# Optimization experiments

Hardware: AMD Instinct MI355X
Metric: run time of the kernel (lower is better)

The kernel has to match this reference:

```python
import jax, jax.numpy as jnp
import numpy as np

B = 32
NC = 10
EPS = 1e-5

# TensorConvLayer2d is modeled as: spatial kh x kw conv over the (H,W)=(32,32) map,
# where each kernel tap applies a bilinear inner-tensor transform U @ T @ V
# (U: [out_t, in_t] on rows, V: [in_t, out_t] on cols), summed over in_channels,
# plus an inner-tensor bias. out_type=0 (fcn_head) contracts the inner tensor to a
# scalar per pixel per output class. TensorBatchNorm2d(18*18) normalizes each of the
# 324 inner-tensor positions over (batch, H, W) with affine gamma/beta (train-mode stats).

def bn(x, g, b):
    # x: (B,H,W,18,18); stats over (B,H,W) per inner position
    m = jnp.mean(x, axis=(0, 1, 2), keepdims=True)
    v = jnp.var(x, axis=(0, 1, 2), keepdims=True)
    return g * (x - m) * jax.lax.rsqrt(v + EPS) + b

def prelu(x, a):
    return jnp.where(x >= 0, x, a * x)

def conv1x1(x, U, V, b):
    # x: (B,H,W,18,18); U,V,b: (18,18)
    return jnp.einsum('bhwpq,ap,qd->bhwad', x, U, V) + b

def conv3x3(x, U, V, b):
    # x: (B,H,W,18,18); U,V: (3,3,18,18); b: (18,18); pad=1, stride=1 on (H,W)
    H, W = x.shape[1], x.shape[2]
    xp = jnp.pad(x, ((0, 0), (1, 1), (1, 1), (0, 0), (0, 0)))
    acc = 0.0
    for i in range(3):
        for j in range(3):
            acc = acc + jnp.einsum('bhwpq,ap,qd->bhwad', xp[:, i:i + H, j:j + W], U[i, j], V[i, j])
    return acc + b

def conv_f0(x, U0, V0, b0):
    # x: (B,8,H,W,16,16) -> (B,H,W,18,18); U0: (8,3,3,18,16), V0: (8,3,3,16,18)
    H, W = x.shape[2], x.shape[3]
    xp = jnp.pad(x, ((0, 0), (0, 0), (1, 1), (1, 1), (0, 0), (0, 0)))
    acc = 0.0
    for i in range(3):
        for j in range(3):
            acc = acc + jnp.einsum('bchwpq,cap,cqd->bhwad', xp[:, :, i:i + H, j:j + W], U0[:, i, j], V0[:, i, j])
    return acc + b0

def _forward(x, U0, V0, b0, U1, V1, b1, U3, V3, b3, Wf, bf, gamma, beta, alpha):
    x = x.reshape(-1, 8, 16, 16, 32, 32).transpose(0, 1, 4, 5, 2, 3)  # (B,8,32,32,16,16)
    h = prelu(bn(conv_f0(x, U0, V0, b0), gamma[0], beta[0]), alpha[0])  # f0

    def resblock(h, i1, i3, ibn, ia):
        t = prelu(bn(conv1x1(h, U1[i1], V1[i1], b1[i1]), gamma[ibn], beta[ibn]), alpha[ia])
        t = prelu(bn(conv3x3(t, U3[i3], V3[i3], b3[i3]), gamma[ibn + 1], beta[ibn + 1]), alpha[ia + 1])
        t = bn(conv1x1(t, U1[i1 + 1], V1[i1 + 1], b1[i1 + 1]), gamma[ibn + 2], beta[ibn + 2])
        return t

    identity = bn(conv1x1(h, U1[0], V1[0], b1[0]), gamma[1], beta[1])      # s1
    x11 = resblock(h, 1, 0, 2, 1) + identity                                # block11
    identity = bn(conv1x1(x11, U1[3], V1[3], b1[3]), gamma[5], beta[5])    # s2
    x21 = resblock(x11, 4, 1, 6, 3) + identity                              # block21
    _dentity = bn(conv1x1(x21, U1[6], V1[6], b1[6]), gamma[9], beta[9])    # s3: typo in source -> unused
    x31 = resblock(x21, 7, 2, 10, 5) + identity                             # bug-faithful: reuses s2 identity
    out = jnp.einsum('bhwpq,opq->bohw', x31, Wf) + bf[None, :, None, None]  # fcn_head, out_type=0
    return out  # (B, NC, 32, 32)

def setup_inputs():
    key = jax.random.key(0)
    ks = jax.random.split(key, 12)
    s = 0.1
    return dict(
        x=jax.random.normal(ks[0], (B, 8, 16, 16, 32, 32), jnp.float32),
        U0=jax.random.normal(ks[1], (8, 3, 3, 18, 16), jnp.float32) * s,
        V0=jax.random.normal(ks[2], (8, 3, 3, 16, 18), jnp.float32) * s,
        b0=jax.random.normal(ks[3], (18, 18), jnp.float32) * s,
        U1=jax.random.normal(ks[4], (9, 18, 18), jnp.float32) * s,
        V1=jax.random.normal(ks[5], (9, 18, 18), jnp.float32) * s,
        b1=jax.random.normal(ks[6], (9, 18, 18), jnp.float32) * s,
        U3=jax.random.normal(ks[7], (3, 3, 3, 18, 18), jnp.float32) * s,
        V3=jax.random.normal(ks[8], (3, 3, 3, 18, 18), jnp.float32) * s,
        b3=jax.random.normal(ks[9], (3, 18, 18), jnp.float32) * s,
        Wf=jax.random.normal(ks[10], (NC, 18, 18), jnp.float32) * s,
        bf=jnp.zeros((NC,), jnp.float32),
        gamma=jnp.ones((13, 18, 18), jnp.float32),
        beta=jnp.zeros((13, 18, 18), jnp.float32),
        alpha=jnp.full((7,), 0.25, jnp.float32),
    )

def reference(x, U0, V0, b0, U1, V1, b1, U3, V3, b3, Wf, bf, gamma, beta, alpha):
    return _forward(x, U0, V0, b0, U1, V1, b1, U3, V3, b3, Wf, bf, gamma, beta, alpha)
```

## Files before the change

kernel.cpp:

```cpp
#include <hip/hip_runtime.h>


#define NPOS 324
#define NPIX 32768
#define NELEM 10616832
#define NF4   2654208

typedef __attribute__((ext_vector_type(8))) short short8;
typedef __attribute__((ext_vector_type(4))) float f32x4;
typedef __attribute__((ext_vector_type(4))) unsigned short us4;

#define AS1 __attribute__((address_space(1)))
#define AS3 __attribute__((address_space(3)))

__device__ __forceinline__ void atomicAddF(float* p, float v) {
    __hip_atomic_fetch_add(p, v, __ATOMIC_RELAXED, __HIP_MEMORY_SCOPE_AGENT);
}
__device__ __forceinline__ unsigned short f2b(float f) {
    unsigned u = __builtin_bit_cast(unsigned, f);
    u = u + 0x7fffu + ((u >> 16) & 1u);
    return (unsigned short)(u >> 16);
}

__global__ __launch_bounds__(512, 2) void k_gconv(
    const unsigned short* __restrict__ in,
    const unsigned short* __restrict__ W,
    float* __restrict__ out,
    float* __restrict__ stats,
    const unsigned short* __restrict__ zb,
    const int KS, const int Kper, const int ntaps)
{
    __shared__ __align__(16) unsigned short Ab[8192];
    __shared__ __align__(16) unsigned short Bb[21504];
    __shared__ float slds[672];

    const int tid = threadIdx.x;
    const int wv  = tid >> 6;
    const int L   = tid & 63;
    const int q   = L >> 4;
    const int l15 = L & 15;
    const int wm  = wv >> 2;
    const int wn  = wv & 3;
    const int ntcnt = (wn == 0) ? 6 : 5;
    const int nt0   = (wn == 0) ? 0 : 6 + 5 * (wn - 1);

    const int blk  = blockIdx.x;
    const int pix0 = blk * 128;
    const int b    = blk >> 3;
    const int h0   = (blk & 7) * 4;

    for (int i = tid; i < 672; i += 512) slds[i] = 0.f;

    const f32x4 fzero = {0.f, 0.f, 0.f, 0.f};
    f32x4 acc[4][6];
#pragma unroll
    for (int i = 0; i < 4; ++i)
#pragma unroll
        for (int j = 0; j < 6; ++j) acc[i][j] = fzero;

    const int nstage = Kper >> 6;
    const int kgper  = Kper >> 3;

    for (int tap = 0; tap < ntaps; ++tap) {
        const int di = (ntaps == 1) ? 0 : (tap / 3 - 1);
        const int dj = (ntaps == 1) ? 0 : (tap % 3 - 1);
        for (int stage = 0; stage < nstage; ++stage) {
            const int kc0 = stage << 6;
#pragma unroll
            for (int is = 0; is < 2; ++is) {
                const int c = wv * 128 + is * 64 + L;
                const int m = c >> 3;
                const int g = (c & 7) ^ (m & 7);
                const int rl = m >> 5;
                const int w  = m & 31;
                const int hin = h0 + rl + di;
                const int win = w + dj;
                const unsigned short* gp;
                if ((unsigned)hin < 32u && (unsigned)win < 32u) {
                    const int pixin = (b * 32 + hin) * 32 + win;
                    gp = in + (size_t)pixin * KS + kc0 + g * 8;
                } else {
                    gp = zb + g * 8;
                }
                __builtin_amdgcn_global_load_lds(
                    (AS1 unsigned short*)(uintptr_t)gp,
                    (AS3 unsigned short*)(Ab + (wv * 128 + is * 64) * 8),
                    16, 0, 0);
            }
            {
                const unsigned short* wbase =
                    W + (size_t)(tap * kgper + stage * 8) * 336 * 8;
#pragma unroll
                for (int it = 0; it < 6; ++it) {
                    const int cb = it * 512 + tid;
                    if (cb < 2688) {
                        __builtin_amdgcn_global_load_lds(
                            (AS1 unsigned short*)(uintptr_t)(wbase + (size_t)cb * 8),
                            (AS3 unsigned short*)(Bb + (it * 512 + wv * 64) * 8),
                            16, 0, 0);
                    }
                }
            }
            __syncthreads();
#pragma unroll
            for (int ks = 0; ks < 2; ++ks) {
                const int g = ks * 4 + q;
                short8 a[4];
#pragma unroll
                for (int i = 0; i < 4; ++i) {
                    const int m = (wm * 4 + i) * 16 + l15;
                    const int slot = (m << 3) + (g ^ (m & 7));
                    a[i] = *(const short8*)(Ab + slot * 8);
                }
                short8 bfr[6];
#pragma unroll
                for (int j = 0; j < 6; ++j)
                    if (j < ntcnt)
                        bfr[j] = *(const short8*)(Bb + ((size_t)g * 336 + (nt0 + j) * 16 + l15) * 8);
#pragma unroll
                for (int i = 0; i < 4; ++i)
#pragma unroll
                    for (int j = 0; j < 6; ++j)
                        if (j < ntcnt)
                            acc[i][j] = __builtin_amdgcn_mfma_f32_16x16x32_bf16(
                                a[i], bfr[j], acc[i][j], 0, 0, 0);
            }
            __syncthreads();
        }
    }
#pragma unroll
    for (int j = 0; j < 6; ++j) {
        if (j < ntcnt) {
            const int n = (nt0 + j) * 16 + l15;
            float s1 = 0.f, s2 = 0.f;
#pragma unroll
            for (int i = 0; i < 4; ++i) {
#pragma unroll
                for (int r = 0; r < 4; ++r) {
                    const float v = acc[i][j][r];
                    s1 += v; s2 += v * v;
                    const int pix = pix0 + (wm * 4 + i) * 16 + q * 4 + r;
                    if (n < NPOS) out[(size_t)pix * NPOS + n] = v;
                }
            }
            s1 += __shfl_xor(s1, 16); s1 += __shfl_xor(s1, 32);
            s2 += __shfl_xor(s2, 16); s2 += __shfl_xor(s2, 32);
            if (L < 16 && n < NPOS) {
                atomicAdd(&slds[n], s1);
                atomicAdd(&slds[336 + n], s2);
            }
        }
    }
    __syncthreads();
    for (int i = tid; i < 648; i += 512) {
        const int rowi = i / 324, n = i - rowi * 324;
        atomicAddF(&stats[rowi * 324 + n], slds[rowi * 336 + n]);
    }
}

__global__ __launch_bounds__(256) void k_xr(
    const float* __restrict__ x, unsigned short* __restrict__ Xr)
{
    __shared__ float Xs[256 * 33];
    const int t = threadIdx.x;
    const int blk = blockIdx.x;
    const int y = blk & 31;
    const int bc = blk >> 5;
    const int c = bc & 7;
    const int bi = bc >> 3;
    const float* xb = x + (size_t)bc * 262144;
    {
        const int w = t & 31, ph = t >> 5;
        for (int it = 0; it < 32; ++it) {
            const int pq = it * 8 + ph;
            Xs[pq * 33 + w] = xb[(size_t)pq * 1024 + y * 32 + w];
        }
    }
    __syncthreads();
    const int w = t >> 3, gg = t & 7;
    unsigned short* orow = Xr + ((size_t)((bi * 32 + y) * 32 + w)) * 2048 + c * 256;
#pragma unroll
    for (int sub = 0; sub < 4; ++sub) {
        const int pq0 = gg * 32 + sub * 8;
        short8 o;
#pragma unroll
        for (int e = 0; e < 8; ++e) o[e] = (short)f2b(Xs[(pq0 + e) * 33 + w]);
        *(short8*)(orow + pq0) = o;
    }
}

__global__ __launch_bounds__(256) void k_pw0(
    const float* __restrict__ U0, const float* __restrict__ V0,
    unsigned short* __restrict__ Wp)
{
    const int t = blockIdx.x * 256 + threadIdx.x;
    if (t >= 9 * 256 * 336) return;
    const int n = t % 336;
    const int kgg = (t / 336) & 255;
    const int tap = t / (336 * 256);
    short8 o = {0, 0, 0, 0, 0, 0, 0, 0};
    if (n < NPOS) {
        const int aa = n / 18, d = n % 18;
#pragma unroll
        for (int j = 0; j < 8; ++j) {
            const int k = kgg * 8 + j;
            const int c = k >> 8, p = (k >> 4) & 15, qq = k & 15;
            const float u = U0[((size_t)(c * 9 + tap) * 18 + aa) * 16 + p];
            const float v = V0[((size_t)(c * 9 + tap) * 16 + qq) * 18 + d];
            o[j] = (short)f2b(u * v);
        }
    }
    *(short8*)(Wp + (size_t)t * 8) = o;
}

__global__ __launch_bounds__(256) void k_pw1(
    const float* __restrict__ U1, const float* __restrict__ V1,
    unsigned short* __restrict__ Wp)
{
    const int t = blockIdx.x * 256 + threadIdx.x;
    if (t >= 9 * 48 * 336) return;
    const int n = t % 336;
    const int kgg = (t / 336) % 48;
    const int cv = t / (336 * 48);
    short8 o = {0, 0, 0, 0, 0, 0, 0, 0};
    if (n < NPOS) {
        const int aa = n / 18, d = n % 18;
#pragma unroll
        for (int j = 0; j < 8; ++j) {
            const int k = kgg * 8 + j;
            if (k < NPOS) {
                const int p = k / 18, qq = k % 18;
                o[j] = (short)f2b(U1[cv * 324 + aa * 18 + p] * V1[cv * 324 + qq * 18 + d]);
            }
        }
    }
    *(short8*)(Wp + (size_t)t * 8) = o;
}

__global__ __launch_bounds__(256) void k_pw3(
    const float* __restrict__ U3, const float* __restrict__ V3,
    unsigned short* __restrict__ Wp)
{
    const int t = blockIdx.x * 256 + threadIdx.x;
    if (t >= 27 * 48 * 336) return;
    const int n = t % 336;
    const int kgg = (t / 336) % 48;
    const int e = t / (336 * 48);
    short8 o = {0, 0, 0, 0, 0, 0, 0, 0};
    if (n < NPOS) {
        const int aa = n / 18, d = n % 18;
#pragma unroll
        for (int j = 0; j < 8; ++j) {
            const int k = kgg * 8 + j;
            if (k < NPOS) {
                const int p = k / 18, qq = k % 18;
                o[j] = (short)f2b(U3[(size_t)e * 324 + aa * 18 + p] * V3[(size_t)e * 324 + qq * 18 + d]);
            }
        }
    }
    *(short8*)(Wp + (size_t)t * 8) = o;
}

__global__ __launch_bounds__(256) void k_apply(
    float* __restrict__ buf, const float* __restrict__ st,
    const float* __restrict__ gamma, const float* __restrict__ beta,
    const float* __restrict__ alpha, const int aidx,
    const float* __restrict__ res,
    unsigned short* __restrict__ bfout)
{
    __shared__ float sc[NPOS], sh[NPOS];
    const int t = threadIdx.x;
    for (int i = t; i < NPOS; i += 256) {
        const float m = st[i] * (1.f / 32768.f);
        float v = st[NPOS + i] * (1.f / 32768.f) - m * m;
        v = fmaxf(v, 0.f);
        const float s = gamma[i] * rsqrtf(v + 1e-5f);
        sc[i] = s;
        sh[i] = beta[i] - m * s;
    }
    __syncthreads();
    const float a = (aidx >= 0) ? alpha[aidx] : 0.f;
    float4* buf4 = (float4*)buf;
    const float4* res4 = (const float4*)res;
    for (int i4 = blockIdx.x * 256 + t; i4 < NF4; i4 += gridDim.x * 256) {
        const float4 v = buf4[i4];
        const int pix = i4 / 81;
        const int pos = (i4 - pix * 81) * 4;
        float rx = sc[pos + 0] * v.x + sh[pos + 0];
        float ry = sc[pos + 1] * v.y + sh[pos + 1];
        float rz = sc[pos + 2] * v.z + sh[pos + 2];
        float rw = sc[pos + 3] * v.w + sh[pos + 3];
        if (aidx >= 0) {
            rx = rx >= 0.f ? rx : a * rx;
            ry = ry >= 0.f ? ry : a * ry;
            rz = rz >= 0.f ? rz : a * rz;
            rw = rw >= 0.f ? rw : a * rw;
        }
        if (res4) {
            const float4 r = res4[i4];
            rx += r.x; ry += r.y; rz += r.z; rw += r.w;
        }
        float4 o; o.x = rx; o.y = ry; o.z = rz; o.w = rw;
        buf4[i4] = o;
        if (bfout) {
            us4 ob = { f2b(rx), f2b(ry), f2b(rz), f2b(rw) };
            *(us4*)(bfout + (size_t)pix * 384 + pos) = ob;
        }
    }
    if (bfout) {
        const us4 z = {0, 0, 0, 0};
        for (int idx = blockIdx.x * 256 + t; idx < NPIX * 15; idx += gridDim.x * 256) {
            const int pix = idx / 15, grp = idx - pix * 15;
            *(us4*)(bfout + (size_t)pix * 384 + 324 + grp * 4) = z;
        }
    }
}

__global__ __launch_bounds__(320) void k_head(
    const float* __restrict__ in, const float* __restrict__ Wf,
    const float* __restrict__ bfv, float* __restrict__ out)
{
    __shared__ float Ts[32 * 325];
    const int t = threadIdx.x;
    const int bh = blockIdx.x;
    const int b = bh >> 5, h = bh & 31;
    const float* src = in + (size_t)bh * (32 * NPOS);
    for (int k = t; k < 32 * NPOS; k += 320)
        Ts[(k / NPOS) * 325 + (k % NPOS)] = src[k];
    __syncthreads();
    const int o = t >> 5, w = t & 31;
    float s = bfv[o];
    const float* wrow = Wf + o * NPOS;
    const float* trow = Ts + w * 325;
#pragma unroll 4
    for (int k = 0; k < NPOS; ++k) s += trow[k] * wrow[k];
    out[(size_t)((b * 10 + o) * 32 + h) * 32 + w] = s;
}

extern "C" void kernel_launch(void* const* d_in, const int* in_sizes, int n_in,
                              void* d_out, int out_size, void* d_ws, size_t ws_size,
                              hipStream_t stream)
{
    (void)in_sizes; (void)n_in; (void)out_size; (void)ws_size;
    const float* x  = (const float*)d_in[0];
    const float* U0 = (const float*)d_in[1];
    const float* V0 = (const float*)d_in[2];
    const float* U1 = (const float*)d_in[4];
    const float* V1 = (const float*)d_in[5];
    const float* U3 = (const float*)d_in[7];
    const float* V3 = (const float*)d_in[8];
    const float* Wf = (const float*)d_in[10];
    const float* bf = (const float*)d_in[11];
    const float* g  = (const float*)d_in[12];
    const float* be = (const float*)d_in[13];
    const float* al = (const float*)d_in[14];
    float* out = (float*)d_out;

    float* A  = (float*)d_ws;
    float* Bu = A  + NELEM;
    float* C  = Bu + NELEM;
    float* D  = C  + NELEM;
    float* st = D  + NELEM;
    unsigned short* XB  = (unsigned short*)(st + 13 * 648);
    unsigned short* TB  = XB + (size_t)NPIX * 384;
    unsigned short* Xr  = TB + (size_t)NPIX * 384;
    unsigned short* W0p = Xr + (size_t)NPIX * 2048;
    unsigned short* W1p = W0p + (size_t)9 * 256 * 336 * 8;
    unsigned short* W3p = W1p + (size_t)9 * 48 * 336 * 8;
    unsigned short* ZB  = W3p + (size_t)27 * 48 * 336 * 8;

    hipMemsetAsync(st, 0, 13 * 648 * sizeof(float), stream);
    hipMemsetAsync(ZB, 0, 4096, stream);

    k_xr<<<8192, 256, 0, stream>>>(x, Xr);
    k_pw0<<<(9 * 256 * 336) / 256, 256, 0, stream>>>(U0, V0, W0p);
    k_pw1<<<(9 * 48 * 336 + 255) / 256, 256, 0, stream>>>(U1, V1, W1p);
    k_pw3<<<(27 * 48 * 336 + 255) / 256, 256, 0, stream>>>(U3, V3, W3p);

    #define ST(k) (st + (k) * 648)
    #define G(k)  (g  + (k) * NPOS)
    #define BE(k) (be + (k) * NPOS)
    #define W1C(k) (W1p + (size_t)(k) * 48 * 336 * 8)
    #define W3C(k) (W3p + (size_t)(k) * 9 * 48 * 336 * 8)

    k_gconv<<<256, 512, 0, stream>>>(Xr, W0p, A, ST(0), ZB, 2048, 2048, 9);
    k_apply<<<1024, 256, 0, stream>>>(A, ST(0), G(0), BE(0), al, 0, nullptr, XB);
    k_gconv<<<256, 512, 0, stream>>>(XB, W1C(0), Bu, ST(1), ZB, 384, 384, 1);
    k_apply<<<1024, 256, 0, stream>>>(Bu, ST(1), G(1), BE(1), al, -1, nullptr, nullptr);
    k_gconv<<<256, 512, 0, stream>>>(XB, W1C(1), C, ST(2), ZB, 384, 384, 1);
    k_apply<<<1024, 256, 0, stream>>>(C, ST(2), G(2), BE(2), al, 1, nullptr, TB);
    k_gconv<<<256, 512, 0, stream>>>(TB, W3C(0), D, ST(3), ZB, 384, 384, 9);
    k_apply<<<1024, 256, 0, stream>>>(D, ST(3), G(3), BE(3), al, 2, nullptr, TB);
    k_gconv<<<256, 512, 0, stream>>>(TB, W1C(2), C, ST(4), ZB, 384, 384, 1);
    k_apply<<<1024, 256, 0, stream>>>(C, ST(4), G(4), BE(4), al, -1, Bu, XB);
    k_gconv<<<256, 512, 0, stream>>>(XB, W1C(3), Bu, ST(5), ZB, 384, 384, 1);
    k_apply<<<1024, 256, 0, stream>>>(Bu, ST(5), G(5), BE(5), al, -1, nullptr, nullptr);
    k_gconv<<<256, 512, 0, stream>>>(XB, W1C(4), A, ST(6), ZB, 384, 384, 1);
    k_apply<<<1024, 256, 0, stream>>>(A, ST(6), G(6), BE(6), al, 3, nullptr, TB);
    k_gconv<<<256, 512, 0, stream>>>(TB, W3C(1), D, ST(7), ZB, 384, 384, 9);
    k_apply<<<1024, 256, 0, stream>>>(D, ST(7), G(7), BE(7), al, 4, nullptr, TB);
    k_gconv<<<256, 512, 0, stream>>>(TB, W1C(5), A, ST(8), ZB, 384, 384, 1);
    k_apply<<<1024, 256, 0, stream>>>(A, ST(8), G(8), BE(8), al, -1, Bu, XB);
    k_gconv<<<256, 512, 0, stream>>>(XB, W1C(7), C, ST(10), ZB, 384, 384, 1);
    k_apply<<<1024, 256, 0, stream>>>(C, ST(10), G(10), BE(10), al, 5, nullptr, TB);
    k_gconv<<<256, 512, 0, stream>>>(TB, W3C(2), D, ST(11), ZB, 384, 384, 9);
    k_apply<<<1024, 256, 0, stream>>>(D, ST(11), G(11), BE(11), al, 6, nullptr, TB);
    k_gconv<<<256, 512, 0, stream>>>(TB, W1C(8), C, ST(12), ZB, 384, 384, 1);
    k_apply<<<1024, 256, 0, stream>>>(C, ST(12), G(12), BE(12), al, -1, Bu, nullptr);
    k_head<<<1024, 320, 0, stream>>>(C, Wf, bf, out);

    #undef ST
    #undef G
    #undef BE
    #undef W1C
    #undef W3C
}
```

Before: 1.915 ms.

## Store conv outputs as bf16, halo-tile 3x3 convs, fuse residual BN into apply

The GEMM conv kernel now uses 256-thread blocks over 64 pixels. It stages the input tile once per K-stage, with a 34-wide halo for 3x3 convs, so all nine taps reuse the same LDS tile, and it double-buffers the A tile. Weights are read straight from global memory instead of LDS. Raw conv outputs are written as bf16 instead of fp32, and a new k_applyR applies batch-norm to both the main and shortcut branches and adds them in one pass, removing the fp32 intermediate buffers. This cuts memory traffic but adds bf16 rounding on the pre-BN activations, and the uncached per-lane weight reads from global memory may slow the MFMA loop.

Result: faster. 1.611 ms (-15.9%).

```diff
diff --git a/kernel.cpp b/kernel.cpp
--- a/kernel.cpp
+++ b/kernel.cpp
@@ -3,12 +3,10 @@
 
 #define NPOS 324
 #define NPIX 32768
-#define NELEM 10616832
-#define NF4   2654208
 
 typedef __attribute__((ext_vector_type(8))) short short8;
+typedef __attribute__((ext_vector_type(8))) unsigned short us8;
 typedef __attribute__((ext_vector_type(4))) float f32x4;
-typedef __attribute__((ext_vector_type(4))) unsigned short us4;
 
 #define AS1 __attribute__((address_space(1)))
 #define AS3 __attribute__((address_space(3)))
@@ -21,17 +19,20 @@
     u = u + 0x7fffu + ((u >> 16) & 1u);
     return (unsigned short)(u >> 16);
 }
-
-__global__ __launch_bounds__(512, 2) void k_gconv(
+__device__ __forceinline__ float b2f(unsigned short h) {
+    unsigned u = ((unsigned)h) << 16;
+    return __builtin_bit_cast(float, u);
+}
+
+__global__ __launch_bounds__(256, 2) void k_gconv(
     const unsigned short* __restrict__ in,
     const unsigned short* __restrict__ W,
-    float* __restrict__ out,
+    unsigned short* __restrict__ raw,
     float* __restrict__ stats,
     const unsigned short* __restrict__ zb,
     const int KS, const int Kper, const int ntaps)
 {
-    __shared__ __align__(16) unsigned short Ab[8192];
-    __shared__ __align__(16) unsigned short Bb[21504];
+    __shared__ __align__(16) unsigned short Ab[2][1088 * 8];
     __shared__ float slds[672];
 
     const int tid = threadIdx.x;
@@ -39,17 +40,20 @@
     const int L   = tid & 63;
     const int q   = L >> 4;
     const int l15 = L & 15;
-    const int wm  = wv >> 2;
-    const int wn  = wv & 3;
+    const int wn  = wv;
     const int ntcnt = (wn == 0) ? 6 : 5;
     const int nt0   = (wn == 0) ? 0 : 6 + 5 * (wn - 1);
 
     const int blk  = blockIdx.x;
-    const int pix0 = blk * 128;
-    const int b    = blk >> 3;
-    const int h0   = (blk & 7) * 4;
-
-    for (int i = tid; i < 672; i += 512) slds[i] = 0.f;
+    const int pix0 = blk * 64;
+    const int b    = blk >> 4;
+    const int h0   = (blk & 15) * 2;
+    const bool halo = (ntaps != 1);
+    const int nchunk = halo ? 1088 : 512;
+    const int nstage = Kper >> 6;
+    const int kgper  = Kper >> 3;
+
+    for (int i = tid; i < 672; i += 256) slds[i] = 0.f;
 
     const f32x4 fzero = {0.f, 0.f, 0.f, 0.f};
     f32x4 acc[4][6];
@@ -58,65 +62,65 @@
 #pragma unroll
         for (int j = 0; j < 6; ++j) acc[i][j] = fzero;
 
-    const int nstage = Kper >> 6;
-    const int kgper  = Kper >> 3;
-
-    for (int tap = 0; tap < ntaps; ++tap) {
-        const int di = (ntaps == 1) ? 0 : (tap / 3 - 1);
-        const int dj = (ntaps == 1) ? 0 : (tap % 3 - 1);
-        for (int stage = 0; stage < nstage; ++stage) {
-            const int kc0 = stage << 6;
-#pragma unroll
-            for (int is = 0; is < 2; ++is) {
-                const int c = wv * 128 + is * 64 + L;
-                const int m = c >> 3;
-                const int g = (c & 7) ^ (m & 7);
-                const int rl = m >> 5;
-                const int w  = m & 31;
-                const int hin = h0 + rl + di;
-                const int win = w + dj;
-                const unsigned short* gp;
-                if ((unsigned)hin < 32u && (unsigned)win < 32u) {
-                    const int pixin = (b * 32 + hin) * 32 + win;
-                    gp = in + (size_t)pixin * KS + kc0 + g * 8;
-                } else {
-                    gp = zb + g * 8;
-                }
-                __builtin_amdgcn_global_load_lds(
-                    (AS1 unsigned short*)(uintptr_t)gp,
-                    (AS3 unsigned short*)(Ab + (wv * 128 + is * 64) * 8),
-                    16, 0, 0);
-            }
-            {
-                const unsigned short* wbase =
-                    W + (size_t)(tap * kgper + stage * 8) * 336 * 8;
-#pragma unroll
-                for (int it = 0; it < 6; ++it) {
-                    const int cb = it * 512 + tid;
-                    if (cb < 2688) {
-                        __builtin_amdgcn_global_load_lds(
-                            (AS1 unsigned short*)(uintptr_t)(wbase + (size_t)cb * 8),
-                            (AS3 unsigned short*)(Bb + (it * 512 + wv * 64) * 8),
-                            16, 0, 0);
-                    }
-                }
-            }
-            __syncthreads();
+#define STAGE_A(sbuf, kc0_)                                                    \
+    for (int it = 0; it < 5; ++it) {                                           \
+        const int c = it * 256 + tid;                                          \
+        if (c < nchunk) {                                                      \
+            const int pixp = c >> 3;                                           \
+            const int g = (c & 7) ^ (pixp & 7);                                \
+            const unsigned short* gp;                                          \
+            if (halo) {                                                        \
+                const int hr = pixp / 34, wc = pixp - hr * 34;                 \
+                const int hh = h0 + hr - 1, ww = wc - 1;                       \
+                if ((unsigned)hh < 32u && (unsigned)ww < 32u)                  \
+                    gp = in + (size_t)((b * 32 + hh) * 32 + ww) * KS + (kc0_) + g * 8; \
+                else                                                           \
+                    gp = zb + g * 8;                                           \
+            } else {                                                           \
+                gp = in + (size_t)(pix0 + pixp) * KS + (kc0_) + g * 8;         \
+            }                                                                  \
+            __builtin_amdgcn_global_load_lds(                                  \
+                (AS1 const unsigned short*)(uintptr_t)gp,                      \
+                (AS3 unsigned short*)(&Ab[sbuf][0] + (it * 256 + wv * 64) * 8),\
+                16, 0, 0);                                                     \
+        }                                                                      \
+    }
+
+    STAGE_A(0, 0)
+    __syncthreads();
+
+    for (int stage = 0; stage < nstage; ++stage) {
+        const int cur = stage & 1;
+        if (stage + 1 < nstage) {
+            STAGE_A(1 - cur, (stage + 1) << 6)
+        }
+        for (int tap = 0; tap < ntaps; ++tap) {
+            const int di = halo ? (tap / 3 - 1) : 0;
+            const int dj = halo ? (tap % 3 - 1) : 0;
+            const unsigned short* wtap = W + (size_t)(tap * kgper + stage * 8) * 336 * 8;
 #pragma unroll
             for (int ks = 0; ks < 2; ++ks) {
                 const int g = ks * 4 + q;
-                short8 a[4];
-#pragma unroll
-                for (int i = 0; i < 4; ++i) {
-                    const int m = (wm * 4 + i) * 16 + l15;
-                    const int slot = (m << 3) + (g ^ (m & 7));
-                    a[i] = *(const short8*)(Ab + slot * 8);
-                }
                 short8 bfr[6];
 #pragma unroll
                 for (int j = 0; j < 6; ++j)
                     if (j < ntcnt)
-                        bfr[j] = *(const short8*)(Bb + ((size_t)g * 336 + (nt0 + j) * 16 + l15) * 8);
+                        bfr[j] = *(const short8*)(wtap + ((size_t)g * 336 + (nt0 + j) * 16 + l15) * 8);
+                short8 a[4];
+#pragma unroll
+                for (int i = 0; i < 4; ++i) {
+                    const int m = i * 16 + l15;
+                    int pixp;
+                    if (halo) {
+                        const int hr = (m >> 5) + di + 1;
+                        const int wc = (m & 31) + dj + 1;
+                        pixp = hr * 34 + wc;
+                    } else {
+                        pixp = m;
+                    }
+                    const int cell = pixp * 8 + (g ^ (pixp & 7));
+                    a[i] = *(const short8*)(&Ab[cur][0] + cell * 8);
+                }
 #pragma unroll
                 for (int i = 0; i < 4; ++i)
 #pragma unroll
@@ -125,9 +129,11 @@
                             acc[i][j] = __builtin_amdgcn_mfma_f32_16x16x32_bf16(
                                 a[i], bfr[j], acc[i][j], 0, 0, 0);
             }
-            __syncthreads();
-        }
-    }
+        }
+        __syncthreads();
+    }
+#undef STAGE_A
+
 #pragma unroll
     for (int j = 0; j < 6; ++j) {
         if (j < ntcnt) {
@@ -139,8 +145,8 @@
                 for (int r = 0; r < 4; ++r) {
                     const float v = acc[i][j][r];
                     s1 += v; s2 += v * v;
-                    const int pix = pix0 + (wm * 4 + i) * 16 + q * 4 + r;
-                    if (n < NPOS) out[(size_t)pix * NPOS + n] = v;
+                    if (n < NPOS)
+                        raw[(size_t)(pix0 + i * 16 + q * 4 + r) * 384 + n] = f2b(v);
                 }
             }
             s1 += __shfl_xor(s1, 16); s1 += __shfl_xor(s1, 32);
@@ -152,7 +158,7 @@
         }
     }
     __syncthreads();
-    for (int i = tid; i < 648; i += 512) {
+    for (int i = tid; i < 648; i += 256) {
         const int rowi = i / 324, n = i - rowi * 324;
         atomicAddF(&stats[rowi * 324 + n], slds[rowi * 336 + n]);
     }
@@ -261,12 +267,11 @@
     *(short8*)(Wp + (size_t)t * 8) = o;
 }
 
-__global__ __launch_bounds__(256) void k_apply(
-    float* __restrict__ buf, const float* __restrict__ st,
+__global__ __launch_bounds__(256) void k_applyA(
+    const unsigned short* __restrict__ rawp, const float* __restrict__ st,
     const float* __restrict__ gamma, const float* __restrict__ beta,
     const float* __restrict__ alpha, const int aidx,
-    const float* __restrict__ res,
-    unsigned short* __restrict__ bfout)
+    unsigned short* __restrict__ outp)
 {
     __shared__ float sc[NPOS], sh[NPOS];
     const int t = threadIdx.x;
@@ -280,53 +285,87 @@
     }
     __syncthreads();
     const float a = (aidx >= 0) ? alpha[aidx] : 0.f;
-    float4* buf4 = (float4*)buf;
-    const float4* res4 = (const float4*)res;
-    for (int i4 = blockIdx.x * 256 + t; i4 < NF4; i4 += gridDim.x * 256) {
-        const float4 v = buf4[i4];
-        const int pix = i4 / 81;
-        const int pos = (i4 - pix * 81) * 4;
-        float rx = sc[pos + 0] * v.x + sh[pos + 0];
-        float ry = sc[pos + 1] * v.y + sh[pos + 1];
-        float rz = sc[pos + 2] * v.z + sh[pos + 2];
-        float rw = sc[pos + 3] * v.w + sh[pos + 3];
-        if (aidx >= 0) {
-            rx = rx >= 0.f ? rx : a * rx;
-            ry = ry >= 0.f ? ry : a * ry;
-            rz = rz >= 0.f ? rz : a * rz;
-            rw = rw >= 0.f ? rw : a * rw;
-        }
-        if (res4) {
-            const float4 r = res4[i4];
-            rx += r.x; ry += r.y; rz += r.z; rw += r.w;
-        }
-        float4 o; o.x = rx; o.y = ry; o.z = rz; o.w = rw;
-        buf4[i4] = o;
-        if (bfout) {
-            us4 ob = { f2b(rx), f2b(ry), f2b(rz), f2b(rw) };
-            *(us4*)(bfout + (size_t)pix * 384 + pos) = ob;
-        }
-    }
-    if (bfout) {
-        const us4 z = {0, 0, 0, 0};
-        for (int idx = blockIdx.x * 256 + t; idx < NPIX * 15; idx += gridDim.x * 256) {
-            const int pix = idx / 15, grp = idx - pix * 15;
-            *(us4*)(bfout + (size_t)pix * 384 + 324 + grp * 4) = z;
-        }
+    for (int idx = blockIdx.x * 256 + t; idx < NPIX * 48; idx += gridDim.x * 256) {
+        const int grp = idx % 48;
+        const int c0 = grp * 8;
+        us8 o;
+        if (c0 < NPOS) {
+            const us8 x = *(const us8*)(rawp + (size_t)idx * 8);
+#pragma unroll
+            for (int e = 0; e < 8; ++e) {
+                const int col = c0 + e;
+                float r = 0.f;
+                if (col < NPOS) {
+                    const float v = b2f(x[e]);
+                    r = sc[col] * v + sh[col];
+                    if (aidx >= 0) r = r >= 0.f ? r : a * r;
+                }
+                o[e] = f2b(r);
+            }
+        } else {
+            o = (us8){0, 0, 0, 0, 0, 0, 0, 0};
+        }
+        *(us8*)(outp + (size_t)idx * 8) = o;
+    }
+}
+
+__global__ __launch_bounds__(256) void k_applyR(
+    const unsigned short* __restrict__ rawA, const float* __restrict__ stA,
+    const float* __restrict__ gA, const float* __restrict__ bA,
+    const unsigned short* __restrict__ rawB, const float* __restrict__ stB,
+    const float* __restrict__ gB, const float* __restrict__ bB,
+    unsigned short* __restrict__ outp)
+{
+    __shared__ float scA[NPOS], shA[NPOS], scB[NPOS], shB[NPOS];
+    const int t = threadIdx.x;
+    for (int i = t; i < NPOS; i += 256) {
+        float m = stA[i] * (1.f / 32768.f);
+        float v = fmaxf(stA[NPOS + i] * (1.f / 32768.f) - m * m, 0.f);
+        float s = gA[i] * rsqrtf(v + 1e-5f);
+        scA[i] = s; shA[i] = bA[i] - m * s;
+        m = stB[i] * (1.f / 32768.f);
+        v = fmaxf(stB[NPOS + i] * (1.f / 32768.f) - m * m, 0.f);
+        s = gB[i] * rsqrtf(v + 1e-5f);
+        scB[i] = s; shB[i] = bB[i] - m * s;
+    }
+    __syncthreads();
+    for (int idx = blockIdx.x * 256 + t; idx < NPIX * 48; idx += gridDim.x * 256) {
+        const int grp = idx % 48;
+        const int c0 = grp * 8;
+        us8 o;
+        if (c0 < NPOS) {
+            const us8 xa = *(const us8*)(rawA + (size_t)idx * 8);
+            const us8 xb = *(const us8*)(rawB + (size_t)idx * 8);
+#pragma unroll
+            for (int e = 0; e < 8; ++e) {
+                const int col = c0 + e;
+                float r = 0.f;
+                if (col < NPOS) {
+                    r = (scA[col] * b2f(xa[e]) + shA[col])
+                      + (scB[col] * b2f(xb[e]) + shB[col]);
+                }
+                o[e] = f2b(r);
+            }
+        } else {
+            o = (us8){0, 0, 0, 0, 0, 0, 0, 0};
+        }
+        *(us8*)(outp + (size_t)idx * 8) = o;
     }
 }
 
 __global__ __launch_bounds__(320) void k_head(
-    const float* __restrict__ in, const float* __restrict__ Wf,
+    const unsigned short* __restrict__ in, const float* __restrict__ Wf,
     const float* __restrict__ bfv, float* __restrict__ out)
 {
     __shared__ float Ts[32 * 325];
     const int t = threadIdx.x;
     const int bh = blockIdx.x;
     const int b = bh >> 5, h = bh & 31;
-    const float* src = in + (size_t)bh * (32 * NPOS);
-    for (int k = t; k < 32 * NPOS; k += 320)
-        Ts[(k / NPOS) * 325 + (k % NPOS)] = src[k];
+    const unsigned short* src = in + (size_t)bh * 32 * 384;
+    for (int k = t; k < 32 * NPOS; k += 320) {
+        const int pl = k / NPOS, col = k - pl * NPOS;
+        Ts[pl * 325 + col] = b2f(src[(size_t)pl * 384 + col]);
+    }
     __syncthreads();
     const int o = t >> 5, w = t & 31;
     float s = bfv[o];
@@ -356,18 +395,22 @@
     const float* al = (const float*)d_in[14];
     float* out = (float*)d_out;
 
-    float* A  = (float*)d_ws;
-    float* Bu = A  + NELEM;
-    float* C  = Bu + NELEM;
-    float* D  = C  + NELEM;
-    float* st = D  + NELEM;
-    unsigned short* XB  = (unsigned short*)(st + 13 * 648);
-    unsigned short* TB  = XB + (size_t)NPIX * 384;
-    unsigned short* Xr  = TB + (size_t)NPIX * 384;
+    const size_t NB = (size_t)NPIX * 384;
+    float* st = (float*)d_ws;
+    unsigned short* ZB  = (unsigned short*)(st + 13 * 648);
+    unsigned short* Xr  = ZB + 2048;
     unsigned short* W0p = Xr + (size_t)NPIX * 2048;
     unsigned short* W1p = W0p + (size_t)9 * 256 * 336 * 8;
     unsigned short* W3p = W1p + (size_t)9 * 48 * 336 * 8;
-    unsigned short* ZB  = W3p + (size_t)27 * 48 * 336 * 8;
+    unsigned short* Rt   = W3p + (size_t)27 * 48 * 336 * 8;
+    unsigned short* Rid1 = Rt + NB;
+    unsigned short* Rid2 = Rid1 + NB;
+    unsigned short* H    = Rid2 + NB;
+    unsigned short* T    = H + NB;
+    unsigned short* T2   = T + NB;
+    unsigned short* X1   = T2 + NB;
+    unsigned short* X2   = X1 + NB;
+    unsigned short* X3   = X2 + NB;
 
     hipMemsetAsync(st, 0, 13 * 648 * sizeof(float), stream);
     hipMemsetAsync(ZB, 0, 4096, stream);
@@ -383,31 +426,32 @@
     #define W1C(k) (W1p + (size_t)(k) * 48 * 336 * 8)
     #define W3C(k) (W3p + (size_t)(k) * 9 * 48 * 336 * 8)
 
-    k_gconv<<<256, 512, 0, stream>>>(Xr, W0p, A, ST(0), ZB, 2048, 2048, 9);
-    k_apply<<<1024, 256, 0, stream>>>(A, ST(0), G(0), BE(0), al, 0, nullptr, XB);
-    k_gconv<<<256, 512, 0, stream>>>(XB, W1C(0), Bu, ST(1), ZB, 384, 384, 1);
-    k_apply<<<1024, 256, 0, stream>>>(Bu, ST(1), G(1), BE(1), al, -1, nullptr, nullptr);
-    k_gconv<<<256, 512, 0, stream>>>(XB, W1C(1), C, ST(2), ZB, 384, 384, 1);
-    k_apply<<<1024, 256, 0, stream>>>(C, ST(2), G(2), BE(2), al, 1, nullptr, TB);
-    k_gconv<<<256, 512, 0, stream>>>(TB, W3C(0), D, ST(3), ZB, 384, 384, 9);
-    k_apply<<<1024, 256, 0, stream>>>(D, ST(3), G(3), BE(3), al, 2, nullptr, TB);
-    k_gconv<<<256, 512, 0, stream>>>(TB, W1C(2), C, ST(4), ZB, 384, 384, 1);
-    k_apply<<<1024, 256, 0, stream>>>(C, ST(4), G(4), BE(4), al, -1, Bu, XB);
-    k_gconv<<<256, 512, 0, stream>>>(XB, W1C(3), Bu, ST(5), ZB, 384, 384, 1);
-    k_apply<<<1024, 256, 0, stream>>>(Bu, ST(5), G(5), BE(5), al, -1, nullptr, nullptr);
-    k_gconv<<<256, 512, 0, stream>>>(XB, W1C(4), A, ST(6), ZB, 384, 384, 1);
-    k_apply<<<1024, 256, 0, stream>>>(A, ST(6), G(6), BE(6), al, 3, nullptr, TB);
-    k_gconv<<<256, 512, 0, stream>>>(TB, W3C(1), D, ST(7), ZB, 384, 384, 9);
-    k_apply<<<1024, 256, 0, stream>>>(D, ST(7), G(7), BE(7), al, 4, nullptr, TB);
-    k_gconv<<<256, 512, 0, stream>>>(TB, W1C(5), A, ST(8), ZB, 384, 384, 1);
-    k_apply<<<1024, 256, 0, stream>>>(A, ST(8), G(8), BE(8), al, -1, Bu, XB);
-    k_gconv<<<256, 512, 0, stream>>>(XB, W1C(7), C, ST(10), ZB, 384, 384, 1);
-    k_apply<<<1024, 256, 0, stream>>>(C, ST(10), G(10), BE(10), al, 5, nullptr, TB);
-    k_gconv<<<256, 512, 0, stream>>>(TB, W3C(2), D, ST(11), ZB, 384, 384, 9);
-    k_apply<<<1024, 256, 0, stream>>>(D, ST(11), G(11), BE(11), al, 6, nullptr, TB);
-    k_gconv<<<256, 512, 0, stream>>>(TB, W1C(8), C, ST(12), ZB, 384, 384, 1);
-    k_apply<<<1024, 256, 0, stream>>>(C, ST(12), G(12), BE(12), al, -1, Bu, nullptr);
-    k_head<<<1024, 320, 0, stream>>>(C, Wf, bf, out);
+    k_gconv<<<512, 256, 0, stream>>>(Xr, W0p, Rt, ST(0), ZB, 2048, 2048, 9);
+    k_applyA<<<2048, 256, 0, stream>>>(Rt, ST(0), G(0), BE(0), al, 0, H);
+    k_gconv<<<512, 256, 0, stream>>>(H, W1C(0), Rid1, ST(1), ZB, 384, 384, 1);
+    k_gconv<<<512, 256, 0, stream>>>(H, W1C(1), Rt, ST(2), ZB, 384, 384, 1);
+    k_applyA<<<2048, 256, 0, stream>>>(Rt, ST(2), G(2), BE(2), al, 1, T);
+    k_gconv<<<512, 256, 0, stream>>>(T, W3C(0), Rt, ST(3), ZB, 384, 384, 9);
+    k_applyA<<<2048, 256, 0, stream>>>(Rt, ST(3), G(3), BE(3), al, 2, T2);
+    k_gconv<<<512, 256, 0, stream>>>(T2, W1C(2), Rt, ST(4), ZB, 384, 384, 1);
+    k_applyR<<<2048, 256, 0, stream>>>(Rt, ST(4), G(4), BE(4),
+                                       Rid1, ST(1), G(1), BE(1), X1);
+    k_gconv<<<512, 256, 0, stream>>>(X1, W1C(3), Rid2, ST(5), ZB, 384, 384, 1);
+    k_gconv<<<512, 256, 0, stream>>>(X1, W1C(4), Rt, ST(6), ZB, 384, 384, 1);
+    k_applyA<<<2048, 256, 0, stream>>>(Rt, ST(6), G(6), BE(6), al, 3, T);
+    k_gconv<<<512, 256, 0, stream>>>(T, W3C(1), Rt, ST(7), ZB, 384, 384, 9);
+    k_applyA<<<2048, 256, 0, stream>>>(Rt, ST(7), G(7), BE(7), al, 4, T2);
+    k_gconv<<<512, 256, 0, stream>>>(T2, W1C(5), Rt, ST(8), ZB, 384, 384, 1);
+    k_applyR<<<2048, 256, 0, stream>>>(Rt, ST(8), G(8), BE(8),
+                                       Rid2, ST(5), G(5), BE(5), X2);
+    k_gconv<<<512, 256, 0, stream>>>(X2, W1C(7), Rt, ST(10), ZB, 384, 384, 1);
+    k_applyA<<<2048, 256, 0, stream>>>(Rt, ST(10), G(10), BE(10), al, 5, T);
+    k_gconv<<<512, 256, 0, stream>>>(T, W3C(2), Rt, ST(11), ZB, 384, 384, 9);
+    k_applyA<<<2048, 256, 0, stream>>>(Rt, ST(11), G(11), BE(11), al, 6, T2);
+    k_gconv<<<512, 256, 0, stream>>>(T2, W1C(8), Rt, ST(12), ZB, 384, 384, 1);
+    k_applyR<<<2048, 256, 0, stream>>>(Rt, ST(12), G(12), BE(12),
+                                       Rid2, ST(5), G(5), BE(5), X3);
+    k_head<<<1024, 320, 0, stream>>>(X3, Wf, bf, out);
 
     #undef ST
     #undef G
```
